# Performance work log

Measured on AMD Instinct MI355X. Metric: run time of the kernel, lower is better.

Reference implementation:

```python
import jax, jax.numpy as jnp
import numpy as np

T = 4096
D_MODEL = 1024
H = 16          # n_heads
HD = 64         # head_dim = d_model // n_heads
LW = 64         # local_window
LT = 16         # latent_tokens
CHUNK = 32      # remote_chunk_size


def setup_inputs() -> dict:
    key = jax.random.key(0)
    ks = jax.random.split(key, 11)
    s = 0.02
    return {
        "x":  jax.random.normal(ks[0], (T, D_MODEL), dtype=jnp.float32),
        "Wq": jax.random.normal(ks[1], (D_MODEL, D_MODEL), dtype=jnp.float32) * s,
        "bq": jnp.zeros((D_MODEL,), dtype=jnp.float32),
        "Wk": jax.random.normal(ks[2], (D_MODEL, D_MODEL), dtype=jnp.float32) * s,
        "bk": jnp.zeros((D_MODEL,), dtype=jnp.float32),
        "Wv": jax.random.normal(ks[3], (D_MODEL, D_MODEL), dtype=jnp.float32) * s,
        "bv": jnp.zeros((D_MODEL,), dtype=jnp.float32),
        "Wo": jax.random.normal(ks[4], (D_MODEL, D_MODEL), dtype=jnp.float32) * s,
        "bo": jnp.zeros((D_MODEL,), dtype=jnp.float32),
        "Wg": jax.random.normal(ks[5], (H, D_MODEL), dtype=jnp.float32) * s,
        "bg": jnp.zeros((H,), dtype=jnp.float32),
    }


def reference(x, Wq, bq, Wk, bk, Wv, bv, Wo, bo, Wg, bg):
    """Runs prefill: forward_step for each token, returning per-step outputs [T, D_MODEL].

    Local cache = circular FIFO of size LW (append + pop-oldest == ring overwrite;
    softmax is permutation-invariant so slot order is irrelevant).
    Evicted tokens accumulate in pending sums; every CHUNK evictions the mean k/v
    is written into the remote latent ring of size LT (oldest overwritten).
    Attention happens BEFORE appending the current token's k/v, matching the torch code.
    """
    scale = 1.0 / np.sqrt(HD)
    Tn = x.shape[0]
    Q = (x @ Wq.T + bq).reshape(Tn, H, HD)
    K = (x @ Wk.T + bk).reshape(Tn, H, HD)
    V = (x @ Wv.T + bv).reshape(Tn, H, HD)
    G = jax.nn.sigmoid(x @ Wg.T + bg)  # [T, H] simple gate

    z = lambda *s: jnp.zeros(s, dtype=x.dtype)
    init = (z(LW, H, HD), z(LW, H, HD),   # local k/v ring
            z(LT, H, HD), z(LT, H, HD),   # remote k/v ring
            z(H, HD), z(H, HD),           # pending k/v sums
            jnp.int32(0), jnp.int32(0))   # pending count, remote count

    def step(carry, inp):
        lk, lv, rk, rv, pks, pvs, pc, rc = carry
        q, k, v, g, t = inp
        # ---- local attention over filled slots (count = min(t, LW)) ----
        lvalid = jnp.arange(LW) < jnp.minimum(t, LW)
        ls = jnp.einsum('hd,nhd->hn', q, lk) * scale
        ls = jnp.where(lvalid[None, :], ls, -1e30)
        lo = jnp.einsum('hn,nhd->hd', jax.nn.softmax(ls, axis=-1), lv)
        lo = lo * (t > 0)
        # ---- remote (compressed latent) attention ----
        rvalid = jnp.arange(LT) < jnp.minimum(rc, LT)
        rs = jnp.einsum('hd,nhd->hn', q, rk) * scale
        rs = jnp.where(rvalid[None, :], rs, -1e30)
        ro = jnp.einsum('hn,nhd->hd', jax.nn.softmax(rs, axis=-1), rv)
        ro = ro * (rc > 0)
        # ---- gate and combine ----
        gate = g[:, None]
        out = gate * lo + (1.0 - gate) * ro  # [H, HD]
        # ---- append k/v: ring write evicts token t-LW into pending ----
        pos = jnp.mod(t, LW)
        evict = (t >= LW)
        pks = pks + jnp.where(evict, lk[pos], 0.0)
        pvs = pvs + jnp.where(evict, lv[pos], 0.0)
        pc = pc + evict.astype(jnp.int32)
        lk = lk.at[pos].set(k)
        lv = lv.at[pos].set(v)
        # ---- compress pending into remote ring when CHUNK reached ----
        comp = (pc == CHUNK)
        ridx = jnp.mod(rc, LT)
        rk = jnp.where(comp, rk.at[ridx].set(pks / CHUNK), rk)
        rv = jnp.where(comp, rv.at[ridx].set(pvs / CHUNK), rv)
        rc = rc + comp.astype(jnp.int32)
        pks = jnp.where(comp, 0.0, pks)
        pvs = jnp.where(comp, 0.0, pvs)
        pc = jnp.where(comp, 0, pc)
        return (lk, lv, rk, rv, pks, pvs, pc, rc), out

    ts = jnp.arange(Tn, dtype=jnp.int32)
    _, outs = jax.lax.scan(step, init, (Q, K, V, G, ts))
    return outs.reshape(Tn, D_MODEL) @ Wo.T + bo
```

## Files before the change

### kernel.cpp

```cpp
#include <hip/hip_runtime.h>
#include <hip/hip_bf16.h>
#include <math.h>

typedef __attribute__((ext_vector_type(8))) short short8;
typedef __attribute__((ext_vector_type(4))) float f32x4;

#define TT 4096
#define DM 1024
#define NH 16
#define HD 64
#define PSTR 168

typedef __attribute__((address_space(3))) unsigned int lds_u32;
typedef __attribute__((address_space(1))) unsigned int glb_u32;

__device__ __forceinline__ void async_cp16(const void* g, void* l) {
    __builtin_amdgcn_global_load_lds((glb_u32*)g, (lds_u32*)l, 16, 0, 0);
}

__device__ __forceinline__ float bf2f(unsigned short u) {
    union { unsigned int i; float f; } v;
    v.i = (unsigned int)u << 16;
    return v.f;
}

__global__ __launch_bounds__(256) void cast_all(
    const float* __restrict__ x,  const float* __restrict__ wq,
    const float* __restrict__ wk, const float* __restrict__ wv,
    const float* __restrict__ wo, const float* __restrict__ wg,
    __hip_bfloat16* __restrict__ xb,  __hip_bfloat16* __restrict__ wqb,
    __hip_bfloat16* __restrict__ wkb, __hip_bfloat16* __restrict__ wvb,
    __hip_bfloat16* __restrict__ wob, __hip_bfloat16* __restrict__ wgb)
{
    int b = blockIdx.x;
    const float* src;
    __hip_bfloat16* dst;
    size_t base;
    if (b < 4096)      { src = x;  dst = xb;  base = (size_t)b * 1024; }
    else if (b < 5120) { src = wq; dst = wqb; base = (size_t)(b - 4096) * 1024; }
    else if (b < 6144) { src = wk; dst = wkb; base = (size_t)(b - 5120) * 1024; }
    else if (b < 7168) { src = wv; dst = wvb; base = (size_t)(b - 6144) * 1024; }
    else if (b < 8192) { src = wo; dst = wob; base = (size_t)(b - 7168) * 1024; }
    else               { src = wg; dst = wgb; base = (size_t)(b - 8192) * 1024; }
    size_t i = base + (size_t)threadIdx.x * 4;
    float4 v = *(const float4*)(src + i);
    __hip_bfloat16 h0 = (__hip_bfloat16)v.x;
    __hip_bfloat16 h1 = (__hip_bfloat16)v.y;
    __hip_bfloat16 h2 = (__hip_bfloat16)v.z;
    __hip_bfloat16 h3 = (__hip_bfloat16)v.w;
    ushort4 u;
    u.x = *(unsigned short*)&h0;
    u.y = *(unsigned short*)&h1;
    u.z = *(unsigned short*)&h2;
    u.w = *(unsigned short*)&h3;
    *(ushort4*)((unsigned short*)dst + i) = u;
}

template <typename OutT>
__global__ __launch_bounds__(256) void gemm128(
    const __hip_bfloat16* __restrict__ A,
    const __hip_bfloat16* __restrict__ B0, const __hip_bfloat16* __restrict__ B1,
    const __hip_bfloat16* __restrict__ B2,
    const float* __restrict__ c0, const float* __restrict__ c1, const float* __restrict__ c2,
    OutT* __restrict__ O0, OutT* __restrict__ O1, OutT* __restrict__ O2)
{
    const int K = DM;
    const int NT = 32;
    __shared__ __align__(16) unsigned short sA[2 * 128 * 32];
    __shared__ __align__(16) unsigned short sB[2 * 128 * 32];

    const int grp = blockIdx.y >> 3;
    const __hip_bfloat16* B = grp == 0 ? B0 : (grp == 1 ? B1 : B2);
    const float* bias       = grp == 0 ? c0 : (grp == 1 ? c1 : c2);
    OutT* O                 = grp == 0 ? O0 : (grp == 1 ? O1 : O2);

    const int tid  = threadIdx.x;
    const int w    = tid >> 6;
    const int lane = tid & 63;
    const int l16  = lane & 15;
    const int quad = lane >> 4;
    const int rowBase = blockIdx.x * 128;
    const int colBase = (blockIdx.y & 7) * 128;

    const int srow   = lane >> 2;
    const int sswz   = (srow & 3) ^ (srow >> 2);
    const int gchunk = (lane & 3) ^ sswz;
    const __hip_bfloat16* gA = A + (size_t)(rowBase + w * 32 + srow) * K + gchunk * 8;
    const __hip_bfloat16* gB = B + (size_t)(colBase + w * 32 + srow) * K + gchunk * 8;
    unsigned short* lA0 = sA + w * 32 * 32;
    unsigned short* lB0 = sB + w * 32 * 32;

    const int fswz = (l16 & 3) ^ (l16 >> 2);
    const int mrow = (w & 1) * 64;
    const int ncol = (w >> 1) * 64;

    f32x4 acc[4][4];
#pragma unroll
    for (int i = 0; i < 4; ++i)
#pragma unroll
        for (int j = 0; j < 4; ++j) acc[i][j] = (f32x4){0.f, 0.f, 0.f, 0.f};

    async_cp16(gA,                     lA0);
    async_cp16(gA + (size_t)16 * K,    lA0 + 16 * 32);
    async_cp16(gB,                     lB0);
    async_cp16(gB + (size_t)16 * K,    lB0 + 16 * 32);
    async_cp16(gA + 32,                  lA0 + 128 * 32);
    async_cp16(gA + 32 + (size_t)16 * K, lA0 + 128 * 32 + 16 * 32);
    async_cp16(gB + 32,                  lB0 + 128 * 32);
    async_cp16(gB + 32 + (size_t)16 * K, lB0 + 128 * 32 + 16 * 32);

    for (int t = 0; t < NT; ++t) {
        if (t == NT - 1) asm volatile("s_waitcnt vmcnt(0)" ::: "memory");
        else             asm volatile("s_waitcnt vmcnt(4)" ::: "memory");
        __builtin_amdgcn_s_barrier();

        const unsigned short* pA = sA + (t & 1) * (128 * 32);
        const unsigned short* pB = sB + (t & 1) * (128 * 32);
        short8 af[4], bf[4];
#pragma unroll
        for (int mt = 0; mt < 4; ++mt)
            af[mt] = *(const short8*)&pA[(mrow + mt * 16 + l16) * 32 + (quad ^ fswz) * 8];
#pragma unroll
        for (int nt = 0; nt < 4; ++nt)
            bf[nt] = *(const short8*)&pB[(ncol + nt * 16 + l16) * 32 + (quad ^ fswz) * 8];
        asm volatile("s_waitcnt lgkmcnt(0)" ::: "memory");
        __builtin_amdgcn_sched_barrier(0);
        __builtin_amdgcn_s_barrier();

        if (t + 2 < NT) {
            const int k2 = (t + 2) * 32;
            unsigned short* dA = lA0 + (t & 1) * (128 * 32);
            unsigned short* dB = lB0 + (t & 1) * (128 * 32);
            async_cp16(gA + k2,                  dA);
            async_cp16(gA + k2 + (size_t)16 * K, dA + 16 * 32);
            async_cp16(gB + k2,                  dB);
            async_cp16(gB + k2 + (size_t)16 * K, dB + 16 * 32);
        }

#pragma unroll
        for (int mt = 0; mt < 4; ++mt)
#pragma unroll
            for (int nt = 0; nt < 4; ++nt)
                acc[mt][nt] = __builtin_amdgcn_mfma_f32_16x16x32_bf16(af[mt], bf[nt], acc[mt][nt], 0, 0, 0);
    }

#pragma unroll
    for (int nt = 0; nt < 4; ++nt) {
        int col = colBase + ncol + nt * 16 + l16;
        float bv = bias[col];
#pragma unroll
        for (int mt = 0; mt < 4; ++mt) {
#pragma unroll
            for (int r = 0; r < 4; ++r) {
                int row = rowBase + mrow + mt * 16 + quad * 4 + r;
                O[(size_t)row * DM + col] = (OutT)(acc[mt][nt][r] + bv);
            }
        }
    }
}

template <typename OutT>
__global__ __launch_bounds__(256) void gemm_n64(
    const __hip_bfloat16* __restrict__ A,
    const __hip_bfloat16* __restrict__ B,
    const float* __restrict__ bias,
    OutT* __restrict__ O)
{
    const int K = DM;
    const int NT = 32;
    __shared__ __align__(16) unsigned short sA[2 * 128 * 32];
    __shared__ __align__(16) unsigned short sB[2 * 64 * 32];

    const int tid  = threadIdx.x;
    const int w    = tid >> 6;
    const int lane = tid & 63;
    const int l16  = lane & 15;
    const int quad = lane >> 4;
    const int rowBase = blockIdx.x * 128;
    const int colBase = blockIdx.y * 64;

    const int srow   = lane >> 2;
    const int sswz   = (srow & 3) ^ (srow >> 2);
    const int gchunk = (lane & 3) ^ sswz;
    const __hip_bfloat16* gA = A + (size_t)(rowBase + w * 32 + srow) * K + gchunk * 8;
    const __hip_bfloat16* gB = B + (size_t)(colBase + w * 16 + srow) * K + gchunk * 8;
    unsigned short* lA0 = sA + w * 32 * 32;
    unsigned short* lB0 = sB + w * 16 * 32;

    const int fswz = (l16 & 3) ^ (l16 >> 2);
    const int mrow = w * 32;

    f32x4 acc[2][4];
#pragma unroll
    for (int i = 0; i < 2; ++i)
#pragma unroll
        for (int j = 0; j < 4; ++j) acc[i][j] = (f32x4){0.f, 0.f, 0.f, 0.f};

    async_cp16(gA,                  lA0);
    async_cp16(gA + (size_t)16 * K, lA0 + 16 * 32);
    async_cp16(gB,                  lB0);
    async_cp16(gA + 32,                  lA0 + 128 * 32);
    async_cp16(gA + 32 + (size_t)16 * K, lA0 + 128 * 32 + 16 * 32);
    async_cp16(gB + 32,                  lB0 + 64 * 32);

    for (int t = 0; t < NT; ++t) {
        if (t == NT - 1) asm volatile("s_waitcnt vmcnt(0)" ::: "memory");
        else             asm volatile("s_waitcnt vmcnt(3)" ::: "memory");
        __builtin_amdgcn_s_barrier();

        const unsigned short* pA = sA + (t & 1) * (128 * 32);
        const unsigned short* pB = sB + (t & 1) * (64 * 32);
        short8 af[2], bf[4];
#pragma unroll
        for (int mt = 0; mt < 2; ++mt)
            af[mt] = *(const short8*)&pA[(mrow + mt * 16 + l16) * 32 + (quad ^ fswz) * 8];
#pragma unroll
        for (int nt = 0; nt < 4; ++nt)
            bf[nt] = *(const short8*)&pB[(nt * 16 + l16) * 32 + (quad ^ fswz) * 8];
        asm volatile("s_waitcnt lgkmcnt(0)" ::: "memory");
        __builtin_amdgcn_sched_barrier(0);
        __builtin_amdgcn_s_barrier();

        if (t + 2 < NT) {
            const int k2 = (t + 2) * 32;
            unsigned short* dA = lA0 + (t & 1) * (128 * 32);
            unsigned short* dB = lB0 + (t & 1) * (64 * 32);
            async_cp16(gA + k2,                  dA);
            async_cp16(gA + k2 + (size_t)16 * K, dA + 16 * 32);
            async_cp16(gB + k2,                  dB);
        }

#pragma unroll
        for (int mt = 0; mt < 2; ++mt)
#pragma unroll
            for (int nt = 0; nt < 4; ++nt)
                acc[mt][nt] = __builtin_amdgcn_mfma_f32_16x16x32_bf16(af[mt], bf[nt], acc[mt][nt], 0, 0, 0);
    }

#pragma unroll
    for (int nt = 0; nt < 4; ++nt) {
        int col = colBase + nt * 16 + l16;
        float bv = bias[col];
#pragma unroll
        for (int mt = 0; mt < 2; ++mt) {
#pragma unroll
            for (int r = 0; r < 4; ++r) {
                int row = rowBase + mrow + mt * 16 + quad * 4 + r;
                O[(size_t)row * DM + col] = (OutT)(acc[mt][nt][r] + bv);
            }
        }
    }
}

__global__ __launch_bounds__(256) void aux_kernel(
    const __hip_bfloat16* __restrict__ K,
    const __hip_bfloat16* __restrict__ V,
    const __hip_bfloat16* __restrict__ xb,
    const __hip_bfloat16* __restrict__ Wgb,
    const float* __restrict__ bg,
    __hip_bfloat16* __restrict__ CK,
    __hip_bfloat16* __restrict__ CV,
    float* __restrict__ G)
{
    const int b = blockIdx.x;
    if (b < 256) {
        const int c  = b >> 1;
        const int d0 = (b & 1) * 512 + threadIdx.x * 2;
        const unsigned short* Ku = (const unsigned short*)K;
        const unsigned short* Vu = (const unsigned short*)V;
        float ak0 = 0.f, ak1 = 0.f, av0 = 0.f, av1 = 0.f;
#pragma unroll 8
        for (int i = 0; i < 32; ++i) {
            size_t off = (size_t)(c * 32 + i) * DM + d0;
            ushort2 kv = *(const ushort2*)(Ku + off);
            ushort2 vv = *(const ushort2*)(Vu + off);
            ak0 += bf2f(kv.x); ak1 += bf2f(kv.y);
            av0 += bf2f(vv.x); av1 += bf2f(vv.y);
        }
        __hip_bfloat16 k0 = (__hip_bfloat16)(ak0 * (1.f / 32.f));
        __hip_bfloat16 k1 = (__hip_bfloat16)(ak1 * (1.f / 32.f));
        __hip_bfloat16 v0 = (__hip_bfloat16)(av0 * (1.f / 32.f));
        __hip_bfloat16 v1 = (__hip_bfloat16)(av1 * (1.f / 32.f));
        ushort2 ko, vo;
        ko.x = *(unsigned short*)&k0; ko.y = *(unsigned short*)&k1;
        vo.x = *(unsigned short*)&v0; vo.y = *(unsigned short*)&v1;
        *(ushort2*)((unsigned short*)CK + (size_t)c * DM + d0) = ko;
        *(ushort2*)((unsigned short*)CV + (size_t)c * DM + d0) = vo;
        return;
    }
    const int unit = threadIdx.x >> 6;
    const int lane = threadIdx.x & 63;
    const int l16  = lane & 15;
    const int quad = lane >> 4;
    const int t0   = (b - 256) * 64 + unit * 16;
    const __hip_bfloat16* ap = xb  + (size_t)(t0 + l16) * DM + quad * 8;
    const __hip_bfloat16* bp = Wgb + (size_t)l16 * DM + quad * 8;
    f32x4 acc = (f32x4){0.f, 0.f, 0.f, 0.f};
#pragma unroll 4
    for (int k0 = 0; k0 < DM; k0 += 32) {
        short8 a = *(const short8*)(ap + k0);
        short8 bb = *(const short8*)(bp + k0);
        acc = __builtin_amdgcn_mfma_f32_16x16x32_bf16(a, bb, acc, 0, 0, 0);
    }
    float bgv = bg[l16];
#pragma unroll
    for (int r = 0; r < 4; ++r) {
        int t = t0 + quad * 4 + r;
        float z = acc[r] + bgv;
        G[t * NH + l16] = 1.f / (1.f + __expf(-z));
    }
}

__global__ __launch_bounds__(256) void attn_mfma(
    const __hip_bfloat16* __restrict__ Q,
    const __hip_bfloat16* __restrict__ K,
    const __hip_bfloat16* __restrict__ V,
    const __hip_bfloat16* __restrict__ CK,
    const __hip_bfloat16* __restrict__ CV,
    const float* __restrict__ G,
    __hip_bfloat16* __restrict__ Aout)
{
    __shared__ alignas(16) unsigned short Pls[64 * PSTR];
    __shared__ alignas(16) unsigned short Vts[64 * PSTR];

    const int h   = blockIdx.y;
    const int t0  = blockIdx.x * 64;
    const int tid = threadIdx.x;
    const int w    = tid >> 6;
    const int lane = tid & 63;
    const int l16  = lane & 15;
    const int quad = lane >> 4;
    const float scale = 0.125f;

    const int rc0  = (t0 >= 96) ? ((t0 - 64) >> 5) : 0;
    const int cmin = rc0 > 16 ? rc0 - 16 : 0;

    const unsigned short* Vu  = (const unsigned short*)V;
    const unsigned short* CVu = (const unsigned short*)CV;

    {
#pragma unroll
        for (int gg = 0; gg < 2; ++gg) {
            const int g = w * 2 + gg;
#pragma unroll
            for (int i = 0; i < 2; ++i) {
                const int pair = lane + 64 * i;
                if (pair < 80) {
                    const int j = pair * 2;
                    const unsigned short *s0, *s1;
                    if (j < 128) {
                        int tok0 = t0 - 64 + j; if (tok0 < 0) tok0 = 0;
                        int tok1 = t0 - 63 + j; if (tok1 < 0) tok1 = 0;
                        s0 = Vu + (size_t)tok0 * DM + h * 64 + g * 8;
                        s1 = Vu + (size_t)tok1 * DM + h * 64 + g * 8;
                    } else {
                        int c0 = cmin + (j - 128); if (c0 > 127) c0 = 127;
                        int c1 = c0 + 1;           if (c1 > 127) c1 = 127;
                        s0 = CVu + (size_t)c0 * DM + h * 64 + g * 8;
                        s1 = CVu + (size_t)c1 * DM + h * 64 + g * 8;
                    }
                    short8 v0 = *(const short8*)s0;
                    short8 v1 = *(const short8*)s1;
#pragma unroll
                    for (int e = 0; e < 8; ++e) {
                        ushort2 pk;
                        pk.x = (unsigned short)v0[e];
                        pk.y = (unsigned short)v1[e];
                        *(ushort2*)&Vts[(g * 8 + e) * PSTR + j] = pk;
                    }
                }
            }
        }
    }

    const __hip_bfloat16* qp = Q + (size_t)(t0 + w * 16 + l16) * DM + h * 64 + quad * 8;
    short8 qf0 = *(const short8*)(qp);
    short8 qf1 = *(const short8*)(qp + 32);

    f32x4 sc[8];
#pragma unroll
    for (int jt = 0; jt < 8; ++jt) {
        int j = jt * 16 + l16;
        int tok = t0 - 64 + j;
        tok = tok < 0 ? 0 : tok;
        const __hip_bfloat16* kp = K + (size_t)tok * DM + h * 64 + quad * 8;
        short8 b0 = *(const short8*)(kp);
        short8 b1 = *(const short8*)(kp + 32);
        f32x4 a = __builtin_amdgcn_mfma_f32_16x16x32_bf16(qf0, b0, (f32x4){0.f,0.f,0.f,0.f}, 0, 0, 0);
        sc[jt]  = __builtin_amdgcn_mfma_f32_16x16x32_bf16(qf1, b1, a, 0, 0, 0);
    }
    f32x4 sc2[2];
#pragma unroll
    for (int jt = 0; jt < 2; ++jt) {
        int c = cmin + jt * 16 + l16;
        if (c > 127) c = 127;
        const __hip_bfloat16* cp = CK + (size_t)c * DM + h * 64 + quad * 8;
        short8 b0 = *(const short8*)(cp);
        short8 b1 = *(const short8*)(cp + 32);
        f32x4 a = __builtin_amdgcn_mfma_f32_16x16x32_bf16(qf0, b0, (f32x4){0.f,0.f,0.f,0.f}, 0, 0, 0);
        sc2[jt] = __builtin_amdgcn_mfma_f32_16x16x32_bf16(qf1, b1, a, 0, 0, 0);
    }

    __syncthreads();

    const int rbase = w * 16 + quad * 4;
    float gl[4], g2[4];
    float mx[4], sm[4], mx2[4], sm2[4];
#pragma unroll
    for (int reg = 0; reg < 4; ++reg) {
        int rr = rbase + reg;
        int t  = t0 + rr;
        float g = G[t * NH + h];
        int rc = (t >= 96) ? ((t - 64) >> 5) : 0;
        gl[reg] = (t > 0)  ? g        : 0.f;
        g2[reg] = (rc > 0) ? (1.f - g) : 0.f;

        int jlo = rr > (64 - t0) ? rr : (64 - t0);
        int jhi = rr + 63;
        float m = -1e30f;
#pragma unroll
        for (int jt = 0; jt < 8; ++jt) {
            int j = jt * 16 + l16;
            float s = (j >= jlo && j <= jhi) ? sc[jt][reg] * scale : -1e30f;
            sc[jt][reg] = s;
            m = fmaxf(m, s);
        }
        mx[reg] = m;

        int nvis = rc < 16 ? rc : 16;
        int clo = rc - nvis, chi = rc - 1;
        float m2 = -1e30f;
#pragma unroll
        for (int jt = 0; jt < 2; ++jt) {
            int c = cmin + jt * 16 + l16;
            float s = (c >= clo && c <= chi) ? sc2[jt][reg] * scale : -1e30f;
            sc2[jt][reg] = s;
            m2 = fmaxf(m2, s);
        }
        mx2[reg] = m2;
    }
#pragma unroll
    for (int off = 1; off <= 8; off <<= 1)
#pragma unroll
        for (int reg = 0; reg < 4; ++reg) {
            mx[reg]  = fmaxf(mx[reg],  __shfl_xor(mx[reg],  off));
            mx2[reg] = fmaxf(mx2[reg], __shfl_xor(mx2[reg], off));
        }
#pragma unroll
    for (int reg = 0; reg < 4; ++reg) {
        float s = 0.f, s2 = 0.f;
#pragma unroll
        for (int jt = 0; jt < 8; ++jt) {
            float p = __expf(sc[jt][reg] - mx[reg]);
            sc[jt][reg] = p;
            s += p;
        }
#pragma unroll
        for (int jt = 0; jt < 2; ++jt) {
            float p = __expf(sc2[jt][reg] - mx2[reg]);
            sc2[jt][reg] = p;
            s2 += p;
        }
        sm[reg] = s; sm2[reg] = s2;
    }
#pragma unroll
    for (int off = 1; off <= 8; off <<= 1)
#pragma unroll
        for (int reg = 0; reg < 4; ++reg) {
            sm[reg]  += __shfl_xor(sm[reg],  off);
            sm2[reg] += __shfl_xor(sm2[reg], off);
        }

#pragma unroll
    for (int reg = 0; reg < 4; ++reg) {
        float f1 = gl[reg] / sm[reg];
        float f2 = g2[reg] / sm2[reg];
        int rowoff = (rbase + reg) * PSTR;
#pragma unroll
        for (int jt = 0; jt < 8; ++jt) {
            __hip_bfloat16 hb = (__hip_bfloat16)(sc[jt][reg] * f1);
            Pls[rowoff + jt * 16 + l16] = *(unsigned short*)&hb;
        }
#pragma unroll
        for (int jt = 0; jt < 2; ++jt) {
            __hip_bfloat16 hb = (__hip_bfloat16)(sc2[jt][reg] * f2);
            Pls[rowoff + 128 + jt * 16 + l16] = *(unsigned short*)&hb;
        }
    }
    asm volatile("s_waitcnt lgkmcnt(0)" ::: "memory");

    f32x4 o[4];
#pragma unroll
    for (int nt = 0; nt < 4; ++nt) o[nt] = (f32x4){0.f, 0.f, 0.f, 0.f};
#pragma unroll
    for (int kt = 0; kt < 5; ++kt) {
        short8 a = *(const short8*)&Pls[(w * 16 + l16) * PSTR + kt * 32 + quad * 8];
#pragma unroll
        for (int nt = 0; nt < 4; ++nt) {
            int dd = nt * 16 + l16;
            short8 b = *(const short8*)&Vts[dd * PSTR + kt * 32 + quad * 8];
            o[nt] = __builtin_amdgcn_mfma_f32_16x16x32_bf16(a, b, o[nt], 0, 0, 0);
        }
    }

#pragma unroll
    for (int nt = 0; nt < 4; ++nt) {
#pragma unroll
        for (int reg = 0; reg < 4; ++reg) {
            int row = t0 + rbase + reg;
            int col = h * 64 + nt * 16 + l16;
            Aout[(size_t)row * DM + col] = (__hip_bfloat16)(o[nt][reg]);
        }
    }
}

extern "C" void kernel_launch(void* const* d_in, const int* in_sizes, int n_in,
                              void* d_out, int out_size, void* d_ws, size_t ws_size,
                              hipStream_t stream)
{
    const float* x  = (const float*)d_in[0];
    const float* Wq = (const float*)d_in[1];
    const float* bq = (const float*)d_in[2];
    const float* Wk = (const float*)d_in[3];
    const float* bk = (const float*)d_in[4];
    const float* Wv = (const float*)d_in[5];
    const float* bv = (const float*)d_in[6];
    const float* Wo = (const float*)d_in[7];
    const float* bo = (const float*)d_in[8];
    const float* Wg = (const float*)d_in[9];
    const float* bg = (const float*)d_in[10];
    float* out = (float*)d_out;

    char* ws = (char*)d_ws;
    const size_t MB = 1024 * 1024;
    __hip_bfloat16* xb  = (__hip_bfloat16*)(ws + 0 * MB);
    __hip_bfloat16* Qb  = (__hip_bfloat16*)(ws + 8 * MB);
    __hip_bfloat16* Kb  = (__hip_bfloat16*)(ws + 16 * MB);
    __hip_bfloat16* Vb  = (__hip_bfloat16*)(ws + 24 * MB);
    __hip_bfloat16* Ab  = (__hip_bfloat16*)(ws + 32 * MB);
    __hip_bfloat16* Wqb = (__hip_bfloat16*)(ws + 40 * MB);
    __hip_bfloat16* Wkb = (__hip_bfloat16*)(ws + 42 * MB);
    __hip_bfloat16* Wvb = (__hip_bfloat16*)(ws + 44 * MB);
    __hip_bfloat16* Wob = (__hip_bfloat16*)(ws + 46 * MB);
    __hip_bfloat16* CKb = (__hip_bfloat16*)(ws + 48 * MB);
    __hip_bfloat16* CVb = (__hip_bfloat16*)(ws + 48 * MB + 256*1024);
    float* Gf           = (float*)(ws + 48 * MB + 512 * 1024);
    __hip_bfloat16* Wgb = (__hip_bfloat16*)(ws + 48 * MB + 768*1024);

    cast_all<<<dim3(8208), 256, 0, stream>>>(x, Wq, Wk, Wv, Wo, Wg,
                                             xb, Wqb, Wkb, Wvb, Wob, Wgb);

    gemm128<__hip_bfloat16><<<dim3(32, 24), 256, 0, stream>>>(
        xb, Wqb, Wkb, Wvb, bq, bk, bv, Qb, Kb, Vb);
    aux_kernel<<<dim3(320), 256, 0, stream>>>(Kb, Vb, xb, Wgb, bg, CKb, CVb, Gf);
    attn_mfma<<<dim3(64, 16), 256, 0, stream>>>(Qb, Kb, Vb, CKb, CVb, Gf, Ab);
    gemm_n64<float><<<dim3(32, 16), 256, 0, stream>>>(Ab, Wob, bo, out);
}
```

Measured before the change: 177.4 us.

## Replace QKV GEMM with 256x256-tile, 8-wave kernel and finer-grained load pipelining

The fused QKV projection GEMM moves from 128x128 tiles with 4 waves to 256x256 tiles with 8 waves and a K-step of 64, cutting global/LDS traffic per FLOP. Loads are split into quarter-tile stages interleaved between four MFMA phases, with s_setprio raising priority around the MFMA bursts. The grid shrinks from 768 to 192 blocks, which may underfill the GPU's compute units and uses about 128 KB of LDS per block.

```diff
diff --git a/kernel.cpp b/kernel.cpp
--- a/kernel.cpp
+++ b/kernel.cpp
@@ -57,19 +57,18 @@
 }
 
 template <typename OutT>
-__global__ __launch_bounds__(256) void gemm128(
+__global__ __launch_bounds__(512, 2) void gemm256(
     const __hip_bfloat16* __restrict__ A,
     const __hip_bfloat16* __restrict__ B0, const __hip_bfloat16* __restrict__ B1,
     const __hip_bfloat16* __restrict__ B2,
     const float* __restrict__ c0, const float* __restrict__ c1, const float* __restrict__ c2,
     OutT* __restrict__ O0, OutT* __restrict__ O1, OutT* __restrict__ O2)
 {
-    const int K = DM;
-    const int NT = 32;
-    __shared__ __align__(16) unsigned short sA[2 * 128 * 32];
-    __shared__ __align__(16) unsigned short sB[2 * 128 * 32];
-
-    const int grp = blockIdx.y >> 3;
+    const int K  = DM;
+    const int NT = 16;
+    __shared__ __align__(16) unsigned short sL[2][4][128 * 64];
+
+    const int grp = blockIdx.y >> 2;
     const __hip_bfloat16* B = grp == 0 ? B0 : (grp == 1 ? B1 : B2);
     const float* bias       = grp == 0 ? c0 : (grp == 1 ? c1 : c2);
     OutT* O                 = grp == 0 ? O0 : (grp == 1 ? O1 : O2);
@@ -79,81 +78,126 @@
     const int lane = tid & 63;
     const int l16  = lane & 15;
     const int quad = lane >> 4;
-    const int rowBase = blockIdx.x * 128;
-    const int colBase = (blockIdx.y & 7) * 128;
-
-    const int srow   = lane >> 2;
-    const int sswz   = (srow & 3) ^ (srow >> 2);
-    const int gchunk = (lane & 3) ^ sswz;
-    const __hip_bfloat16* gA = A + (size_t)(rowBase + w * 32 + srow) * K + gchunk * 8;
-    const __hip_bfloat16* gB = B + (size_t)(colBase + w * 32 + srow) * K + gchunk * 8;
-    unsigned short* lA0 = sA + w * 32 * 32;
-    unsigned short* lB0 = sB + w * 32 * 32;
-
-    const int fswz = (l16 & 3) ^ (l16 >> 2);
-    const int mrow = (w & 1) * 64;
-    const int ncol = (w >> 1) * 64;
-
-    f32x4 acc[4][4];
-#pragma unroll
-    for (int i = 0; i < 4; ++i)
+    const int wr   = w >> 2;
+    const int wc   = w & 3;
+    const int rowBase = blockIdx.x * 256;
+    const int colBase = (blockIdx.y & 3) * 256;
+
+    const int srow = lane >> 3;
+    const int schk = (lane & 7) ^ srow;
+    const __hip_bfloat16* gA = A + (size_t)(rowBase + w * 8 + srow) * K + schk * 8;
+    const __hip_bfloat16* gB = B + (size_t)(colBase + w * 8 + srow) * K + schk * 8;
+    const int dstoff = w * 8 * 64;
+
+#define STG(buf, slot, gbase, half, kt) do {                                                   \
+    async_cp16((gbase) + (size_t)((half) * 128)      * K + (kt) * 64, &sL[buf][slot][dstoff]); \
+    async_cp16((gbase) + (size_t)((half) * 128 + 64) * K + (kt) * 64, &sL[buf][slot][64 * 64 + dstoff]); \
+} while (0)
+
+    const int cs0 = ((quad)     ^ (l16 & 7)) * 8;
+    const int cs1 = ((4 + quad) ^ (l16 & 7)) * 8;
+
+    f32x4 acc[8][4];
+#pragma unroll
+    for (int i = 0; i < 8; ++i)
 #pragma unroll
         for (int j = 0; j < 4; ++j) acc[i][j] = (f32x4){0.f, 0.f, 0.f, 0.f};
 
-    async_cp16(gA,                     lA0);
-    async_cp16(gA + (size_t)16 * K,    lA0 + 16 * 32);
-    async_cp16(gB,                     lB0);
-    async_cp16(gB + (size_t)16 * K,    lB0 + 16 * 32);
-    async_cp16(gA + 32,                  lA0 + 128 * 32);
-    async_cp16(gA + 32 + (size_t)16 * K, lA0 + 128 * 32 + 16 * 32);
-    async_cp16(gB + 32,                  lB0 + 128 * 32);
-    async_cp16(gB + 32 + (size_t)16 * K, lB0 + 128 * 32 + 16 * 32);
-
+    STG(0, 2, gB, 0, 0); STG(0, 3, gB, 1, 0); STG(0, 0, gA, 0, 0); STG(0, 1, gA, 1, 0);
+    STG(1, 2, gB, 0, 1); STG(1, 3, gB, 1, 1); STG(1, 0, gA, 0, 1);
+
+    short8 af[4][2], bf[4][2];
     for (int t = 0; t < NT; ++t) {
+        const int b = t & 1;
+        const unsigned short* pa = &sL[b][wr][0];
+        const unsigned short* pb = &sL[b][2 + (wc >> 1)][(wc & 1) * 64 * 64];
+
         if (t == NT - 1) asm volatile("s_waitcnt vmcnt(0)" ::: "memory");
-        else             asm volatile("s_waitcnt vmcnt(4)" ::: "memory");
+        else             asm volatile("s_waitcnt vmcnt(6)" ::: "memory");
         __builtin_amdgcn_s_barrier();
-
-        const unsigned short* pA = sA + (t & 1) * (128 * 32);
-        const unsigned short* pB = sB + (t & 1) * (128 * 32);
-        short8 af[4], bf[4];
-#pragma unroll
-        for (int mt = 0; mt < 4; ++mt)
-            af[mt] = *(const short8*)&pA[(mrow + mt * 16 + l16) * 32 + (quad ^ fswz) * 8];
-#pragma unroll
-        for (int nt = 0; nt < 4; ++nt)
-            bf[nt] = *(const short8*)&pB[(ncol + nt * 16 + l16) * 32 + (quad ^ fswz) * 8];
+#pragma unroll
+        for (int m = 0; m < 4; ++m) {
+            af[m][0] = *(const short8*)&pa[(m * 16 + l16) * 64 + cs0];
+            af[m][1] = *(const short8*)&pa[(m * 16 + l16) * 64 + cs1];
+        }
+#pragma unroll
+        for (int n = 0; n < 2; ++n) {
+            bf[n][0] = *(const short8*)&pb[(n * 16 + l16) * 64 + cs0];
+            bf[n][1] = *(const short8*)&pb[(n * 16 + l16) * 64 + cs1];
+        }
+        if (t + 1 < NT) STG(b ^ 1, 1, gA, 1, t + 1);
         asm volatile("s_waitcnt lgkmcnt(0)" ::: "memory");
         __builtin_amdgcn_sched_barrier(0);
+        __builtin_amdgcn_s_setprio(1);
+#pragma unroll
+        for (int ks = 0; ks < 2; ++ks)
+#pragma unroll
+            for (int m = 0; m < 4; ++m)
+#pragma unroll
+                for (int n = 0; n < 2; ++n)
+                    acc[m][n] = __builtin_amdgcn_mfma_f32_16x16x32_bf16(af[m][ks], bf[n][ks], acc[m][n], 0, 0, 0);
+        __builtin_amdgcn_s_setprio(0);
+
+#pragma unroll
+        for (int n = 2; n < 4; ++n) {
+            bf[n][0] = *(const short8*)&pb[(n * 16 + l16) * 64 + cs0];
+            bf[n][1] = *(const short8*)&pb[(n * 16 + l16) * 64 + cs1];
+        }
+        asm volatile("s_waitcnt lgkmcnt(0)" ::: "memory");
+        __builtin_amdgcn_sched_barrier(0);
+        __builtin_amdgcn_s_setprio(1);
+#pragma unroll
+        for (int ks = 0; ks < 2; ++ks)
+#pragma unroll
+            for (int m = 0; m < 4; ++m)
+#pragma unroll
+            for (int n = 2; n < 4; ++n)
+                acc[m][n] = __builtin_amdgcn_mfma_f32_16x16x32_bf16(af[m][ks], bf[n][ks], acc[m][n], 0, 0, 0);
+        __builtin_amdgcn_s_setprio(0);
         __builtin_amdgcn_s_barrier();
 
-        if (t + 2 < NT) {
-            const int k2 = (t + 2) * 32;
-            unsigned short* dA = lA0 + (t & 1) * (128 * 32);
-            unsigned short* dB = lB0 + (t & 1) * (128 * 32);
-            async_cp16(gA + k2,                  dA);
-            async_cp16(gA + k2 + (size_t)16 * K, dA + 16 * 32);
-            async_cp16(gB + k2,                  dB);
-            async_cp16(gB + k2 + (size_t)16 * K, dB + 16 * 32);
-        }
-
-#pragma unroll
-        for (int mt = 0; mt < 4; ++mt)
-#pragma unroll
-            for (int nt = 0; nt < 4; ++nt)
-                acc[mt][nt] = __builtin_amdgcn_mfma_f32_16x16x32_bf16(af[mt], bf[nt], acc[mt][nt], 0, 0, 0);
-    }
-
-#pragma unroll
-    for (int nt = 0; nt < 4; ++nt) {
-        int col = colBase + ncol + nt * 16 + l16;
+#pragma unroll
+        for (int m = 0; m < 4; ++m) {
+            af[m][0] = *(const short8*)&pa[((m + 4) * 16 + l16) * 64 + cs0];
+            af[m][1] = *(const short8*)&pa[((m + 4) * 16 + l16) * 64 + cs1];
+        }
+        if (t + 2 < NT) STG(b, 2, gB, 0, t + 2);
+        asm volatile("s_waitcnt lgkmcnt(0)" ::: "memory");
+        __builtin_amdgcn_sched_barrier(0);
+        __builtin_amdgcn_s_setprio(1);
+#pragma unroll
+        for (int ks = 0; ks < 2; ++ks)
+#pragma unroll
+            for (int m = 0; m < 4; ++m)
+#pragma unroll
+                for (int n = 0; n < 2; ++n)
+                    acc[m + 4][n] = __builtin_amdgcn_mfma_f32_16x16x32_bf16(af[m][ks], bf[n][ks], acc[m + 4][n], 0, 0, 0);
+        __builtin_amdgcn_s_setprio(0);
+        __builtin_amdgcn_s_barrier();
+
+        if (t + 2 < NT) { STG(b, 3, gB, 1, t + 2); STG(b, 0, gA, 0, t + 2); }
+        __builtin_amdgcn_s_setprio(1);
+#pragma unroll
+        for (int ks = 0; ks < 2; ++ks)
+#pragma unroll
+            for (int m = 0; m < 4; ++m)
+#pragma unroll
+            for (int n = 2; n < 4; ++n)
+                acc[m + 4][n] = __builtin_amdgcn_mfma_f32_16x16x32_bf16(af[m][ks], bf[n][ks], acc[m + 4][n], 0, 0, 0);
+        __builtin_amdgcn_s_setprio(0);
+    }
+#undef STG
+
+#pragma unroll
+    for (int n = 0; n < 4; ++n) {
+        int col = colBase + wc * 64 + n * 16 + l16;
         float bv = bias[col];
 #pragma unroll
-        for (int mt = 0; mt < 4; ++mt) {
+        for (int m = 0; m < 8; ++m) {
 #pragma unroll
             for (int r = 0; r < 4; ++r) {
-                int row = rowBase + mrow + mt * 16 + quad * 4 + r;
-                O[(size_t)row * DM + col] = (OutT)(acc[mt][nt][r] + bv);
+                int row = rowBase + wr * 128 + m * 16 + quad * 4 + r;
+                O[(size_t)row * DM + col] = (OutT)(acc[m][n][r] + bv);
             }
         }
     }
@@ -550,7 +594,7 @@
     cast_all<<<dim3(8208), 256, 0, stream>>>(x, Wq, Wk, Wv, Wo, Wg,
                                              xb, Wqb, Wkb, Wvb, Wob, Wgb);
 
-    gemm128<__hip_bfloat16><<<dim3(32, 24), 256, 0, stream>>>(
+    gemm256<__hip_bfloat16><<<dim3(16, 12), 512, 0, stream>>>(
         xb, Wqb, Wkb, Wvb, bq, bk, bv, Qb, Kb, Vb);
     aux_kernel<<<dim3(320), 256, 0, stream>>>(Kb, Vb, xb, Wgb, bg, CKb, CVb, Gf);
     attn_mfma<<<dim3(64, 16), 256, 0, stream>>>(Qb, Kb, Vb, CKb, CVb, Gf, Ab);
```

After: 177.4 us. Within noise of the previous version (-0.0%).
